# Performance work log

Measured on AMD Instinct MI355X. Metric: run time of the kernel, lower is better.

Reference implementation:

```python
import jax, jax.numpy as jnp
import numpy as np

MAX_STEPS = 8
COMMIT = 0.25
DECAY = 0.99
EPS = 1e-5


def gru_cell(x, h, W_ih, W_hh, b_ih, b_hh):
    # PyTorch GRU cell, gate order (r, z, n)
    gx = x @ W_ih.T + b_ih            # [B, 3H]
    gh = h @ W_hh.T + b_hh            # [B, 3H]
    xr, xz, xn = jnp.split(gx, 3, axis=-1)
    hr, hz, hn = jnp.split(gh, 3, axis=-1)
    r = jax.nn.sigmoid(xr + hr)
    z = jax.nn.sigmoid(xz + hz)
    n = jnp.tanh(xn + r * hn)
    return (1.0 - z) * n + z * h


def setup_inputs() -> dict:
    key = jax.random.key(0)
    ks = jax.random.split(key, 16)
    B, C, Hs, Ws = 1024, 512, 7, 7
    D, K, Hd = 256, 8192, 512
    sc = lambda k, shape, s: (jax.random.normal(k, shape, jnp.float32) * s)
    codebook = jax.random.uniform(ks[14], (K, D), jnp.float32, -1.0 / K, 1.0 / K)
    return {
        "spatial_features": sc(ks[0], (B, C, Hs, Ws), 1.0),
        "bos_token": sc(ks[1], (D,), 0.02),
        "W_ih": sc(ks[2], (3 * Hd, D), 0.05),
        "W_hh": sc(ks[3], (3 * Hd, Hd), 0.05),
        "b_ih": sc(ks[4], (3 * Hd,), 0.05),
        "b_hh": sc(ks[5], (3 * Hd,), 0.05),
        "Wg": sc(ks[6], (C, Hd), 0.02),
        "bg": sc(ks[7], (C,), 0.02),
        "Wb": sc(ks[8], (C, Hd), 0.02),
        "bb": sc(ks[9], (C,), 0.02),
        "W1": sc(ks[10], (Hd, Hd + C), 0.03),
        "b1": sc(ks[11], (Hd,), 0.03),
        "W2": sc(ks[12], (D, Hd), 0.05),
        "b2": sc(ks[13], (D,), 0.05),
        "codebook": codebook,
        "ema_cluster_size": jnp.zeros((K,), jnp.float32),
        "ema_w": codebook,
    }


def reference(spatial_features, bos_token, W_ih, W_hh, b_ih, b_hh,
              Wg, bg, Wb, bb, W1, b1, W2, b2,
              codebook, ema_cluster_size, ema_w):
    B = spatial_features.shape[0]
    K, D = codebook.shape
    Hd = W_hh.shape[1]
    # FiLM + global mean pooling is linear -> fold mean over HxW once.
    # mean((1+g)*F + b) == (1+g)*mean(F) + b  (same math, fewer bytes)
    spatial_mean = spatial_features.mean(axis=(2, 3))  # [B, C]

    def step(carry, _):
        h, prev, cb, cs, ew, loss = carry
        h = gru_cell(prev, h, W_ih, W_hh, b_ih, b_hh)            # [B, Hd]
        gamma = h @ Wg.T + bg
        beta = h @ Wb.T + bb
        c = (1.0 + gamma) * spatial_mean + beta                   # [B, C]
        pin = jnp.concatenate([h, c], axis=-1)                    # [B, Hd+C]
        z = jax.nn.relu(pin @ W1.T + b1) @ W2.T + b2              # [B, D]
        # VQ nearest neighbor (squared L2)
        d = (jnp.sum(z * z, axis=-1, keepdims=True)
             - 2.0 * (z @ cb.T)
             + jnp.sum(cb * cb, axis=-1))                         # [B, K]
        idx = jnp.argmin(d, axis=-1)                              # [B]
        z_q = cb[idx]                                             # [B, D]
        # EMA codebook update (uses OLD codebook for this step's z_q)
        zd = jax.lax.stop_gradient(z)
        counts = jnp.zeros((K,), z.dtype).at[idx].add(1.0)
        dw = jnp.zeros_like(cb).at[idx].add(zd)
        cs = DECAY * cs + (1.0 - DECAY) * counts
        n_tot = cs.sum()
        cs = (cs + EPS) / (n_tot + K * EPS) * n_tot               # Laplace smoothing
        ew = DECAY * ew + (1.0 - DECAY) * dw
        cb_new = ew / cs[:, None]
        vq = COMMIT * jnp.mean((z - jax.lax.stop_gradient(z_q)) ** 2)
        z_q_ste = z + jax.lax.stop_gradient(z_q - z)              # straight-through
        return (h, z_q_ste, cb_new, cs, ew, loss + vq), (z_q_ste, idx, z)

    h0 = jnp.zeros((B, Hd), spatial_features.dtype)
    prev0 = jnp.broadcast_to(bos_token, (B, D))
    init = (h0, prev0, codebook, ema_cluster_size, ema_w, jnp.zeros((), jnp.float32))
    (h_final, _, _, _, _, total_loss), (codes, idxs, zc) = jax.lax.scan(
        step, init, None, length=MAX_STEPS)
    selected_codes = jnp.swapaxes(codes, 0, 1)   # [B, T, D]
    all_indices = jnp.swapaxes(idxs, 0, 1)       # [B, T]
    all_z_cont = jnp.swapaxes(zc, 0, 1)          # [B, T, D]
    avg_vq_loss = total_loss / MAX_STEPS
    return (h_final, selected_codes, all_indices, all_z_cont, avg_vq_loss)
```

## Files before the change

### kernel.cpp

```cpp
#include <hip/hip_runtime.h>

#define BATCH 1024
#define CDIM  512
#define DDIM  256
#define KCB   8192
#define HD    512
#define G3    1536
#define TSTEPS 8

#define WS_CB    ((size_t)0)
#define WS_EW    ((size_t)2097152)
#define WS_CSR   ((size_t)4194304)
#define WS_SM    ((size_t)6291456)
#define WS_H     ((size_t)6815744)
#define WS_PREV  ((size_t)7340032)
#define WS_Z     ((size_t)7602176)
#define WS_GX    ((size_t)7864320)
#define WS_GH    ((size_t)9437184)
#define WS_PIN   ((size_t)12058624)
#define WS_H1    ((size_t)13107200)
#define WS_CS    ((size_t)13631488)
#define WS_CBSQ  ((size_t)13639680)
#define WS_SZZ   ((size_t)13647872)
#define WS_NT    ((size_t)13657088)
#define WS_LOSS  ((size_t)13657090)
#define WS_IDX   ((size_t)13657092)
#define WS_ROWK  ((size_t)13658116)
#define WS_WGWB  ((size_t)13660164)
#define WS_BGBB  ((size_t)14184452)

#define OUT_HF    ((size_t)0)
#define OUT_CODES ((size_t)524288)
#define OUT_IDX   ((size_t)2621440)
#define OUT_ZC    ((size_t)2629632)
#define OUT_LOSS  ((size_t)4726784)

static __device__ __forceinline__ unsigned long long key32(float s, int col) {
  unsigned int u = __float_as_uint(s);
  u = (u & 0x80000000u) ? ~u : (u | 0x80000000u);
  return (((unsigned long long)u) << 32) | (unsigned long long)(unsigned int)col;
}

static __device__ __forceinline__ float pw128(const float* a) {
  float r0=a[0],r1=a[1],r2=a[2],r3=a[3],r4=a[4],r5=a[5],r6=a[6],r7=a[7];
  for (int i = 8; i < 128; i += 8) {
    r0+=a[i+0]; r1+=a[i+1]; r2+=a[i+2]; r3+=a[i+3];
    r4+=a[i+4]; r5+=a[i+5]; r6+=a[i+6]; r7+=a[i+7];
  }
  return ((r0+r1)+(r2+r3))+((r4+r5)+(r6+r7));
}

template<int BM,int BN,int BK,int TM,int TN>
__device__ __forceinline__ void gemm_engine(
    const float* __restrict__ A, int lda,
    const float* __restrict__ B, int ldb, int K,
    int m0, int n0, int tid,
    float* __restrict__ As, float* __restrict__ Bs,
    float (&acc)[TM][TN])
{
  constexpr int NT = 256;
  constexpr int K4 = BK/4;
  constexpr int LA = (BM*BK)/(4*NT);
  constexpr int LB = (BN*BK)/(4*NT);
  constexpr int SA = BM+4;
  constexpr int SB = BN+4;
  constexpr int ACW = (TM % 4 == 0) ? 4 : 2;
  constexpr int BCW = (TN % 4 == 0) ? 4 : 2;
  constexpr int ANC = TM/ACW;
  constexpr int BNC = TN/BCW;
  constexpr int AR  = BM/ANC;
  constexpr int BR  = BN/BNC;
  static_assert((BM/TM)*(BN/TN) == NT, "256 threads");
  static_assert(LA >= 1 && LB >= 1, "stage width");

  const int tx = tid % (BN/TN);
  const int ty = tid / (BN/TN);

  int arow[LA], ak4[LA], brow[LB], bk4[LB];
#pragma unroll
  for (int l=0;l<LA;++l){ int f=l*NT+tid; arow[l]=f/K4; ak4[l]=f%K4; }
#pragma unroll
  for (int l=0;l<LB;++l){ int f=l*NT+tid; brow[l]=f/K4; bk4[l]=f%K4; }

  float4 ra[LA], rb[LB];
#pragma unroll
  for (int l=0;l<LA;++l) ra[l] = *(const float4*)(A + (size_t)(m0+arow[l])*lda + ak4[l]*4);
#pragma unroll
  for (int l=0;l<LB;++l) rb[l] = *(const float4*)(B + (size_t)(n0+brow[l])*ldb + bk4[l]*4);
#pragma unroll
  for (int l=0;l<LA;++l){ int kb=ak4[l]*4, r=arow[l];
    As[(kb+0)*SA+r]=ra[l].x; As[(kb+1)*SA+r]=ra[l].y; As[(kb+2)*SA+r]=ra[l].z; As[(kb+3)*SA+r]=ra[l].w; }
#pragma unroll
  for (int l=0;l<LB;++l){ int kb=bk4[l]*4, r=brow[l];
    Bs[(kb+0)*SB+r]=rb[l].x; Bs[(kb+1)*SB+r]=rb[l].y; Bs[(kb+2)*SB+r]=rb[l].z; Bs[(kb+3)*SB+r]=rb[l].w; }
  __syncthreads();

  int cur = 0;
  for (int k0 = BK; k0 < K; k0 += BK) {
#pragma unroll
    for (int l=0;l<LA;++l) ra[l] = *(const float4*)(A + (size_t)(m0+arow[l])*lda + k0 + ak4[l]*4);
#pragma unroll
    for (int l=0;l<LB;++l) rb[l] = *(const float4*)(B + (size_t)(n0+brow[l])*ldb + k0 + bk4[l]*4);
    {
      const float* as = As + cur*(BK*SA);
      const float* bs = Bs + cur*(BK*SB);
#pragma unroll
      for (int kk=0;kk<BK;++kk){
        float af[TM], bf[TN];
#pragma unroll
        for (int c=0;c<ANC;++c){
          if constexpr (ACW == 4) {
            float4 v = *(const float4*)&as[kk*SA + c*AR + ty*4];
            af[c*4+0]=v.x; af[c*4+1]=v.y; af[c*4+2]=v.z; af[c*4+3]=v.w;
          } else {
            float2 v = *(const float2*)&as[kk*SA + c*AR + ty*2];
            af[c*2+0]=v.x; af[c*2+1]=v.y;
          }
        }
#pragma unroll
        for (int c=0;c<BNC;++c){
          if constexpr (BCW == 4) {
            float4 v = *(const float4*)&bs[kk*SB + c*BR + tx*4];
            bf[c*4+0]=v.x; bf[c*4+1]=v.y; bf[c*4+2]=v.z; bf[c*4+3]=v.w;
          } else {
            float2 v = *(const float2*)&bs[kk*SB + c*BR + tx*2];
            bf[c*2+0]=v.x; bf[c*2+1]=v.y;
          }
        }
#pragma unroll
        for (int i=0;i<TM;++i)
#pragma unroll
          for (int j=0;j<TN;++j) acc[i][j]=fmaf(af[i],bf[j],acc[i][j]);
      }
    }
    {
      float* as = As + (cur^1)*(BK*SA);
      float* bs = Bs + (cur^1)*(BK*SB);
#pragma unroll
      for (int l=0;l<LA;++l){ int kb=ak4[l]*4, r=arow[l];
        as[(kb+0)*SA+r]=ra[l].x; as[(kb+1)*SA+r]=ra[l].y; as[(kb+2)*SA+r]=ra[l].z; as[(kb+3)*SA+r]=ra[l].w; }
#pragma unroll
      for (int l=0;l<LB;++l){ int kb=bk4[l]*4, r=brow[l];
        bs[(kb+0)*SB+r]=rb[l].x; bs[(kb+1)*SB+r]=rb[l].y; bs[(kb+2)*SB+r]=rb[l].z; bs[(kb+3)*SB+r]=rb[l].w; }
    }
    __syncthreads();
    cur ^= 1;
  }
  {
    const float* as = As + cur*(BK*SA);
    const float* bs = Bs + cur*(BK*SB);
#pragma unroll
    for (int kk=0;kk<BK;++kk){
      float af[TM], bf[TN];
#pragma unroll
      for (int c=0;c<ANC;++c){
        if constexpr (ACW == 4) {
          float4 v = *(const float4*)&as[kk*SA + c*AR + ty*4];
          af[c*4+0]=v.x; af[c*4+1]=v.y; af[c*4+2]=v.z; af[c*4+3]=v.w;
        } else {
          float2 v = *(const float2*)&as[kk*SA + c*AR + ty*2];
          af[c*2+0]=v.x; af[c*2+1]=v.y;
        }
      }
#pragma unroll
      for (int c=0;c<BNC;++c){
        if constexpr (BCW == 4) {
          float4 v = *(const float4*)&bs[kk*SB + c*BR + tx*4];
          bf[c*4+0]=v.x; bf[c*4+1]=v.y; bf[c*4+2]=v.z; bf[c*4+3]=v.w;
        } else {
          float2 v = *(const float2*)&bs[kk*SB + c*BR + tx*2];
          bf[c*2+0]=v.x; bf[c*2+1]=v.y;
        }
      }
#pragma unroll
      for (int i=0;i<TM;++i)
#pragma unroll
        for (int j=0;j<TN;++j) acc[i][j]=fmaf(af[i],bf[j],acc[i][j]);
    }
  }
}

__global__ __launch_bounds__(256) void gemm_gxgh_kernel(
    const float* __restrict__ PREV, const float* __restrict__ H,
    const float* __restrict__ Wih, const float* __restrict__ Whh,
    const float* __restrict__ bih, const float* __restrict__ bhh,
    float* __restrict__ GX, float* __restrict__ GH)
{
  __shared__ float As[2*16*(64+4)];
  __shared__ float Bs[2*16*(64+4)];
  const int z = blockIdx.z;
  const float* A   = z ? H   : PREV;
  const float* B   = z ? Whh : Wih;
  const float* bia = z ? bhh : bih;
  float* C         = z ? GH  : GX;
  const int lda    = z ? HD  : DDIM;
  const int m0 = blockIdx.x * 64, n0 = blockIdx.y * 64;
  float acc[4][4] = {};
  gemm_engine<64,64,16,4,4>(A, lda, B, lda, lda, m0, n0, threadIdx.x, As, Bs, acc);
  {
#pragma clang fp contract(off)
    const int tx = threadIdx.x & 15, ty = threadIdx.x >> 4;
#pragma unroll
    for (int i = 0; i < 4; ++i)
#pragma unroll
      for (int j = 0; j < 4; ++j)
        C[(size_t)(m0 + ty*4 + i) * G3 + n0 + tx*4 + j] = acc[i][j] + bia[n0 + tx*4 + j];
  }
}

__global__ __launch_bounds__(256) void gemm_gb_film_kernel(
    const float* __restrict__ H, const float* __restrict__ W,
    const float* __restrict__ bv, const float* __restrict__ SM,
    float* __restrict__ PIN)
{
  __shared__ float As[2*32*(32+4)];
  __shared__ float Bs[2*32*(64+4)];
  const int m0 = blockIdx.x * 32, n0 = blockIdx.y * 64;
  float acc[2][4] = {};
  gemm_engine<32,64,32,2,4>(H, HD, W, HD, HD, m0, n0, threadIdx.x, As, Bs, acc);
  {
#pragma clang fp contract(off)
    const int tx = threadIdx.x & 15, ty = threadIdx.x >> 4;
    const int cb0 = n0 + tx * 4;
#pragma unroll
    for (int i = 0; i < 2; ++i) {
      const int row = m0 + ty*2 + i;
#pragma unroll
      for (int p = 0; p < 2; ++p) {
        float g  = acc[i][2*p]   + bv[cb0 + 2*p];
        float be = acc[i][2*p+1] + bv[cb0 + 2*p + 1];
        const int ch = (cb0 >> 1) + p;
        float t1 = 1.0f + g;
        float t2 = t1 * SM[(size_t)row * CDIM + ch];
        PIN[(size_t)row * 1024 + 512 + ch] = t2 + be;
      }
    }
  }
}

template<bool RELU,int BM,int BN,int BK,int TM,int TN>
__global__ __launch_bounds__(256) void gemm_mlp_kernel(
    const float* __restrict__ A, int lda,
    const float* __restrict__ B,
    const float* __restrict__ bias, int K, int N, float* __restrict__ C)
{
  __shared__ float As[2*BK*(BM+4)];
  __shared__ float Bs[2*BK*(BN+4)];
  const int m0 = blockIdx.x * BM, n0 = blockIdx.y * BN;
  float acc[TM][TN] = {};
  gemm_engine<BM,BN,BK,TM,TN>(A, lda, B, K, K, m0, n0, threadIdx.x, As, Bs, acc);
  {
#pragma clang fp contract(off)
    constexpr int ACW = (TM % 4 == 0) ? 4 : 2;
    constexpr int BCW = (TN % 4 == 0) ? 4 : 2;
    constexpr int AR  = BM/(TM/ACW);
    constexpr int BR  = BN/(TN/BCW);
    const int tx = threadIdx.x % (BN/TN), ty = threadIdx.x / (BN/TN);
#pragma unroll
    for (int i = 0; i < TM; ++i) {
      const int row = m0 + (i/ACW)*AR + ty*ACW + (i%ACW);
#pragma unroll
      for (int j = 0; j < TN; ++j) {
        const int col = n0 + (j/BCW)*BR + tx*BCW + (j%BCW);
        float v = acc[i][j] + bias[col];
        if (RELU) v = fmaxf(v, 0.0f);
        C[(size_t)row * N + col] = v;
      }
    }
  }
}

__global__ __launch_bounds__(256) void gemm_score_argmin(
    const float* __restrict__ A,
    const float* __restrict__ Bc,
    const float* __restrict__ cbsq,
    const float* __restrict__ szz,
    unsigned long long* __restrict__ rowkeys)
{
  __shared__ float As[16][68];
  __shared__ float Bs[16][68];
  __shared__ unsigned long long Ks[64][17];
  const int tid = threadIdx.x;
  const int tx = tid & 15, ty = tid >> 4;
  const int fid = blockIdx.x + (blockIdx.y << 4);
  const int xcd = fid & 7;
  const int loc = fid >> 3;
  const int m0 = (loc & 15) * 64;
  const int n0 = ((xcd << 4) + (loc >> 4)) * 64;
  const int lr = tid >> 2, lq = tid & 3;
  const float4* Ab = (const float4*)(A + (size_t)(m0 + lr) * DDIM);
  const float4* Bb = (const float4*)(Bc + (size_t)(n0 + lr) * DDIM);
  float acc[4][4] = {};
  for (int k0 = 0; k0 < DDIM; k0 += 16) {
    float4 av = Ab[(k0 >> 2) + lq];
    float4 bv = Bb[(k0 >> 2) + lq];
    __syncthreads();
    As[lq*4+0][lr] = av.x; As[lq*4+1][lr] = av.y;
    As[lq*4+2][lr] = av.z; As[lq*4+3][lr] = av.w;
    Bs[lq*4+0][lr] = bv.x; Bs[lq*4+1][lr] = bv.y;
    Bs[lq*4+2][lr] = bv.z; Bs[lq*4+3][lr] = bv.w;
    __syncthreads();
#pragma unroll
    for (int kk = 0; kk < 16; ++kk) {
      float4 a = *(const float4*)&As[kk][ty*4];
      float4 b = *(const float4*)&Bs[kk][tx*4];
      acc[0][0]=fmaf(a.x,b.x,acc[0][0]); acc[0][1]=fmaf(a.x,b.y,acc[0][1]); acc[0][2]=fmaf(a.x,b.z,acc[0][2]); acc[0][3]=fmaf(a.x,b.w,acc[0][3]);
      acc[1][0]=fmaf(a.y,b.x,acc[1][0]); acc[1][1]=fmaf(a.y,b.y,acc[1][1]); acc[1][2]=fmaf(a.y,b.z,acc[1][2]); acc[1][3]=fmaf(a.y,b.w,acc[1][3]);
      acc[2][0]=fmaf(a.z,b.x,acc[2][0]); acc[2][1]=fmaf(a.z,b.y,acc[2][1]); acc[2][2]=fmaf(a.z,b.z,acc[2][2]); acc[2][3]=fmaf(a.z,b.w,acc[2][3]);
      acc[3][0]=fmaf(a.w,b.x,acc[3][0]); acc[3][1]=fmaf(a.w,b.y,acc[3][1]); acc[3][2]=fmaf(a.w,b.z,acc[3][2]); acc[3][3]=fmaf(a.w,b.w,acc[3][3]);
    }
  }
  {
#pragma clang fp contract(off)
    const int nb = n0 + tx * 4;
#pragma unroll
    for (int i = 0; i < 4; ++i) {
      float sz = szz[m0 + ty*4 + i];
      unsigned long long kb[4];
#pragma unroll
      for (int j = 0; j < 4; ++j) {
        float g2 = 2.0f * acc[i][j];
        float t1 = sz - g2;
        float d  = t1 + cbsq[nb + j];
        kb[j] = key32(d, nb + j);
      }
      unsigned long long ka = kb[0] < kb[1] ? kb[0] : kb[1];
      unsigned long long kc = kb[2] < kb[3] ? kb[2] : kb[3];
      Ks[ty*4 + i][tx] = ka < kc ? ka : kc;
    }
  }
  __syncthreads();
  if (tid < 64) {
    unsigned long long best = Ks[tid][0];
#pragma unroll
    for (int t = 1; t < 16; ++t) {
      unsigned long long v = Ks[tid][t];
      best = v < best ? v : best;
    }
    atomicMin(&rowkeys[m0 + tid], best);
  }
}

__global__ __launch_bounds__(256) void pw256_rows_kernel(const float* __restrict__ src,
                                                         float* __restrict__ dst,
                                                         int square) {
#pragma clang fp contract(off)
  int gid = blockIdx.x * 256 + threadIdx.x;
  int row = gid >> 4;
  int l = gid & 15;
  const float* a = src + (size_t)row * 256 + ((l >> 3) << 7) + (l & 7);
  float v0 = a[0];
  float r = square ? v0 * v0 : v0;
  for (int i = 1; i < 16; ++i) {
    float w = a[i << 3];
    r += square ? w * w : w;
  }
  float t = r + __shfl_xor(r, 1);
  t = t + __shfl_xor(t, 2);
  t = t + __shfl_xor(t, 4);
  float s = t + __shfl_xor(t, 8);
  if (l == 0) dst[row] = s;
}

__global__ __launch_bounds__(256) void smean_kernel(const float* __restrict__ sf,
                                                    float* __restrict__ sm) {
#pragma clang fp contract(off)
  int i = blockIdx.x * 256 + threadIdx.x;
  const float* a = sf + (size_t)i * 49;
  float r0=a[0],r1=a[1],r2=a[2],r3=a[3],r4=a[4],r5=a[5],r6=a[6],r7=a[7];
  for (int k = 8; k < 48; k += 8) {
    r0+=a[k+0]; r1+=a[k+1]; r2+=a[k+2]; r3+=a[k+3];
    r4+=a[k+4]; r5+=a[k+5]; r6+=a[k+6]; r7+=a[k+7];
  }
  float res = ((r0+r1)+(r2+r3))+((r4+r5)+(r6+r7));
  res += a[48];
  sm[i] = res / 49.0f;
}

__global__ __launch_bounds__(256) void previnit_kernel(const float* __restrict__ bos,
                                                       float* __restrict__ prev) {
  int i = blockIdx.x * 256 + threadIdx.x;
  prev[i] = bos[i & (DDIM - 1)];
}

__global__ __launch_bounds__(256) void interleave_film_kernel(
    const float* __restrict__ Wg, const float* __restrict__ Wb,
    const float* __restrict__ bg, const float* __restrict__ bb,
    float* __restrict__ W, float* __restrict__ bv) {
  int i = blockIdx.x * 256 + threadIdx.x;
  int row = i >> 9, k = i & 511;
  const float* src = (row & 1) ? Wb : Wg;
  W[i] = src[(size_t)(row >> 1) * 512 + k];
  if (i < 1024) bv[i] = ((i & 1) ? bb : bg)[i >> 1];
}

__global__ __launch_bounds__(256) void gru_kernel(const float* __restrict__ gx,
                                                  const float* __restrict__ gh,
                                                  float* __restrict__ h,
                                                  float* __restrict__ pin) {
#pragma clang fp contract(off)
  int i = blockIdx.x * 256 + threadIdx.x;
  int b = i >> 9, j = i & 511;
  size_t o = (size_t)b * G3;
  float xr = gx[o + j], xz = gx[o + 512 + j], xn = gx[o + 1024 + j];
  float hr = gh[o + j], hz = gh[o + 512 + j], hn = gh[o + 1024 + j];
  float ar = xr + hr;
  float az = xz + hz;
  float er = expf(-ar);
  float ez = expf(-az);
  float r  = 1.0f / (1.0f + er);
  float zz = 1.0f / (1.0f + ez);
  float rh = r * hn;
  float an = xn + rh;
  float n  = tanhf(an);
  float hold = h[i];
  float t1 = (1.0f - zz) * n;
  float t2 = zz * hold;
  float hnew = t1 + t2;
  h[i] = hnew;
  pin[(size_t)b * 1024 + j] = hnew;
}

__global__ __launch_bounds__(256) void vq_apply_kernel(
    unsigned long long* __restrict__ rowkeys,
    const float* __restrict__ cb, const float* __restrict__ zbuf,
    float* __restrict__ prev, int* __restrict__ idxarr,
    float* __restrict__ loss_acc, float* __restrict__ out, int t)
{
#pragma clang fp contract(off)
  int b = blockIdx.x, d = threadIdx.x;
  int idx = (int)(rowkeys[b] & 0xFFFFFFFFull);
  float zq = cb[(size_t)idx * DDIM + d];
  float zb = zbuf[(size_t)b * DDIM + d];
  float delta = zq - zb;
  float zste = zb + delta;
  size_t td = ((size_t)b * TSTEPS + t) * DDIM + d;
  out[OUT_CODES + td] = zste;
  out[OUT_ZC + td] = zb;
  prev[(size_t)b * DDIM + d] = zste;
  if (d == 0) {
    idxarr[b] = idx;
    out[OUT_IDX + (size_t)b * TSTEPS + t] = (float)idx;
  }
  float diff = zb - zq;
  __shared__ float red[256];
  red[d] = diff * diff; __syncthreads();
  for (int s = 128; s > 0; s >>= 1) { if (d < s) red[d] += red[d + s]; __syncthreads(); }
  if (d == 0) {
    atomicAdd(loss_acc, red[0]);
    rowkeys[b] = ~0ULL;
  }
}

__global__ __launch_bounds__(1024) void csr_cs_kernel(const int* __restrict__ idxarr,
                                                      int* __restrict__ list,
                                                      int* __restrict__ base,
                                                      int* __restrict__ cnts,
                                                      float* __restrict__ cs,
                                                      float* __restrict__ nt) {
  __shared__ __align__(16) int sidx[BATCH];
  __shared__ int scnt[KCB];
  __shared__ int spart[1024];
  __shared__ float scs[KCB];
  __shared__ float s64v[64];
  const int t = threadIdx.x;
  sidx[t] = idxarr[t];
  for (int i = t; i < KCB; i += 1024) scnt[i] = 0;
  __syncthreads();
  const int my = sidx[t];
  atomicAdd(&scnt[my], 1);
  int rank = 0;
  {
    int b = 0;
    for (; b + 4 <= t; b += 4) {
      int4 v = *(const int4*)&sidx[b];
      rank += (v.x == my) + (v.y == my) + (v.z == my) + (v.w == my);
    }
    for (; b < t; ++b) rank += (sidx[b] == my) ? 1 : 0;
  }
  __syncthreads();
  const int c0 = t * 8;
  int loc[8]; int s0 = 0;
#pragma unroll
  for (int i = 0; i < 8; ++i) { loc[i] = s0; s0 += scnt[c0 + i]; }
  spart[t] = s0;
  __syncthreads();
  for (int off = 1; off < 1024; off <<= 1) {
    int v = (t >= off) ? spart[t - off] : 0;
    __syncthreads();
    spart[t] += v;
    __syncthreads();
  }
  {
    int incl = spart[t];
    __syncthreads();
    spart[t] = incl - s0;
    __syncthreads();
  }
  const int off = spart[t];
#pragma unroll
  for (int i = 0; i < 8; ++i) { base[c0 + i] = off + loc[i]; cnts[c0 + i] = scnt[c0 + i]; }
  const int kb = my >> 3, kr = my & 7;
  int bb = spart[kb];
  for (int i = 0; i < kr; ++i) bb += scnt[(kb << 3) + i];
  list[bb + rank] = t;

  {
#pragma clang fp contract(off)
    for (int i = t; i < KCB; i += 1024) {
      float a = 0.99f * cs[i];
      float b2 = 0.01f * (float)scnt[i];
      scs[i] = a + b2;
    }
    __syncthreads();
    if (t < 64) s64v[t] = pw128(scs + t * 128);
    __syncthreads();
    if (t == 0) {
      float v[64];
      for (int i = 0; i < 64; ++i) v[i] = s64v[i];
      for (int len = 64; len > 1; len >>= 1)
        for (int i = 0; i < (len >> 1); ++i) v[i] = v[2*i] + v[2*i+1];
      nt[0] = v[0];
      s64v[0] = v[0];
    }
    __syncthreads();
    const float n = s64v[0];
    const float den = n + 0.08192f;
    for (int i = t; i < KCB; i += 1024) {
      float t1 = scs[i] + 1e-5f;
      float q = t1 / den;
      cs[i] = q * n;
    }
  }
}

__global__ __launch_bounds__(256) void ema_fused_kernel(
    float* __restrict__ ew, const int* __restrict__ list,
    const int* __restrict__ base, const int* __restrict__ cnts,
    const float* __restrict__ zbuf, const float* __restrict__ cs,
    float* __restrict__ cb, float* __restrict__ cbsq)
{
#pragma clang fp contract(off)
  __shared__ float row2[256];
  __shared__ float ch[16];
  const int d = threadIdx.x;
  for (int r = 0; r < 8; ++r) {
    const int k = blockIdx.x * 8 + r;
    const int start = base[k], cnt = cnts[k];
    float acc = 0.0f;
    int i = 0;
    for (; i + 16 <= cnt; i += 16) {
      int bi[16];
#pragma unroll
      for (int u = 0; u < 16; ++u) bi[u] = list[start + i + u];
      float v[16];
#pragma unroll
      for (int u = 0; u < 16; ++u) v[u] = zbuf[(size_t)bi[u] * DDIM + d];
#pragma unroll
      for (int u = 0; u < 16; ++u) acc += v[u];
    }
    for (; i < cnt; ++i) {
      acc += zbuf[(size_t)list[start + i] * DDIM + d];
    }
    const size_t o = (size_t)k * DDIM + d;
    float a = 0.99f * ew[o];
    float bb = 0.01f * acc;
    float e = a + bb;
    ew[o] = e;
    float c = e / cs[k];
    cb[o] = c;
    row2[d] = c * c;
    __syncthreads();
    if (d < 16) {
      int h = d >> 3, j = d & 7;
      const float* p = row2 + h * 128 + j;
      float rr = p[0];
      for (int i2 = 1; i2 < 16; ++i2) rr += p[8 * i2];
      ch[d] = rr;
    }
    __syncthreads();
    if (d == 0) {
      float s0 = ((ch[0]+ch[1])+(ch[2]+ch[3]))+((ch[4]+ch[5])+(ch[6]+ch[7]));
      float s1 = ((ch[8]+ch[9])+(ch[10]+ch[11]))+((ch[12]+ch[13])+(ch[14]+ch[15]));
      cbsq[k] = s0 + s1;
    }
    __syncthreads();
  }
}

__global__ __launch_bounds__(256) void final_kernel(const float* __restrict__ h,
                                                    const float* __restrict__ loss_acc,
                                                    float* __restrict__ out) {
  int i = blockIdx.x * 256 + threadIdx.x;
  out[OUT_HF + i] = h[i];
  if (i == 0)
    out[OUT_LOSS] = 0.25f * (*loss_acc) / ((float)(BATCH * DDIM)) / (float)TSTEPS;
}

extern "C" void kernel_launch(void* const* d_in, const int* in_sizes, int n_in,
                              void* d_out, int out_size, void* d_ws, size_t ws_size,
                              hipStream_t stream) {
  const float* sf    = (const float*)d_in[0];
  const float* bos   = (const float*)d_in[1];
  const float* W_ih  = (const float*)d_in[2];
  const float* W_hh  = (const float*)d_in[3];
  const float* b_ih  = (const float*)d_in[4];
  const float* b_hh  = (const float*)d_in[5];
  const float* Wg    = (const float*)d_in[6];
  const float* bg    = (const float*)d_in[7];
  const float* Wb    = (const float*)d_in[8];
  const float* bb    = (const float*)d_in[9];
  const float* W1    = (const float*)d_in[10];
  const float* b1    = (const float*)d_in[11];
  const float* W2    = (const float*)d_in[12];
  const float* b2    = (const float*)d_in[13];
  const float* cb_in = (const float*)d_in[14];
  const float* cs_in = (const float*)d_in[15];
  const float* ew_in = (const float*)d_in[16];

  float* ws  = (float*)d_ws;
  float* out = (float*)d_out;

  float* CB   = ws + WS_CB;
  float* EW   = ws + WS_EW;
  int*   LIST = (int*)(ws + WS_CSR);
  int*   BASE = LIST + BATCH;
  int*   CNTS = BASE + KCB;
  float* SM   = ws + WS_SM;
  float* H    = ws + WS_H;
  float* PREV = ws + WS_PREV;
  float* Z    = ws + WS_Z;
  float* GX   = ws + WS_GX;
  float* GH   = ws + WS_GH;
  float* PIN  = ws + WS_PIN;
  float* H1   = ws + WS_H1;
  float* CS   = ws + WS_CS;
  float* CBSQ = ws + WS_CBSQ;
  float* SZZ  = ws + WS_SZZ;
  float* NT   = ws + WS_NT;
  float* LOSS = ws + WS_LOSS;
  int*   IDX  = (int*)(ws + WS_IDX);
  unsigned long long* ROWK = (unsigned long long*)(ws + WS_ROWK);
  float* WGWB = ws + WS_WGWB;
  float* BGBB = ws + WS_BGBB;

  (void)hipMemcpyAsync(CB, cb_in, (size_t)KCB * DDIM * 4, hipMemcpyDeviceToDevice, stream);
  (void)hipMemcpyAsync(EW, ew_in, (size_t)KCB * DDIM * 4, hipMemcpyDeviceToDevice, stream);
  (void)hipMemcpyAsync(CS, cs_in, (size_t)KCB * 4, hipMemcpyDeviceToDevice, stream);
  interleave_film_kernel<<<(1024*512)/256, 256, 0, stream>>>(Wg, Wb, bg, bb, WGWB, BGBB);
  (void)hipMemsetAsync(H, 0, (size_t)BATCH * HD * 4, stream);
  (void)hipMemsetAsync(LOSS, 0, 8, stream);
  (void)hipMemsetAsync(ROWK, 0xFF, BATCH * 8, stream);
  previnit_kernel<<<BATCH * DDIM / 256, 256, 0, stream>>>(bos, PREV);
  smean_kernel<<<BATCH * CDIM / 256, 256, 0, stream>>>(sf, SM);
  pw256_rows_kernel<<<(KCB * 16) / 256, 256, 0, stream>>>(CB, CBSQ, 1);

  for (int t = 0; t < TSTEPS; ++t) {
    gemm_gxgh_kernel<<<dim3(BATCH/64, G3/64, 2), 256, 0, stream>>>(
        PREV, H, W_ih, W_hh, b_ih, b_hh, GX, GH);
    gru_kernel<<<BATCH * HD / 256, 256, 0, stream>>>(GX, GH, H, PIN);

    gemm_gb_film_kernel<<<dim3(BATCH/32, 1024/64), 256, 0, stream>>>(H, WGWB, BGBB, SM, PIN);

    gemm_mlp_kernel<true, 64,32,32,4,2><<<dim3(BATCH/64, HD/32),   256, 0, stream>>>(PIN, 1024, W1, b1, 1024, HD, H1);
    gemm_mlp_kernel<false,32,32,32,2,2><<<dim3(BATCH/32, DDIM/32), 256, 0, stream>>>(H1, HD, W2, b2, HD, DDIM, Z);

    pw256_rows_kernel<<<(BATCH * 16) / 256, 256, 0, stream>>>(Z, SZZ, 1);
    gemm_score_argmin<<<dim3(BATCH/64, KCB/64), 256, 0, stream>>>(Z, CB, CBSQ, SZZ, ROWK);
    vq_apply_kernel<<<BATCH, 256, 0, stream>>>(ROWK, CB, Z, PREV, IDX, LOSS, out, t);

    csr_cs_kernel<<<1, 1024, 0, stream>>>(IDX, LIST, BASE, CNTS, CS, NT);
    ema_fused_kernel<<<KCB/8, 256, 0, stream>>>(EW, LIST, BASE, CNTS, Z, CS, CB, CBSQ);
  }

  final_kernel<<<BATCH * HD / 256, 256, 0, stream>>>(H, LOSS, out);
}
```

Baseline: 2.097 ms.

## Rebalance GRU gate GEMM grid and shrink MLP tiles; drop XCD swizzle in score GEMM

The two GRU gate GEMMs now share one flat grid. The input-side GEMM (K=256) keeps 64x64 tiles, while the hidden-side GEMM (K=512) uses 64x32 tiles with a deeper K step, so the longer-K work is split across more blocks. The first MLP GEMM moves to 32x32 tiles to raise the block count. The XCD-aware block remapping in the codebook score/argmin kernel is replaced by a plain 2D block index. Together these aim to improve load balance and occupancy across CUs, but dropping the swizzle may reduce L2 locality for codebook reads.

```diff
diff --git a/kernel.cpp b/kernel.cpp
--- a/kernel.cpp
+++ b/kernel.cpp
@@ -186,25 +186,35 @@
     const float* __restrict__ bih, const float* __restrict__ bhh,
     float* __restrict__ GX, float* __restrict__ GH)
 {
-  __shared__ float As[2*16*(64+4)];
-  __shared__ float Bs[2*16*(64+4)];
-  const int z = blockIdx.z;
-  const float* A   = z ? H   : PREV;
-  const float* B   = z ? Whh : Wih;
-  const float* bia = z ? bhh : bih;
-  float* C         = z ? GH  : GX;
-  const int lda    = z ? HD  : DDIM;
-  const int m0 = blockIdx.x * 64, n0 = blockIdx.y * 64;
-  float acc[4][4] = {};
-  gemm_engine<64,64,16,4,4>(A, lda, B, lda, lda, m0, n0, threadIdx.x, As, Bs, acc);
-  {
-#pragma clang fp contract(off)
-    const int tx = threadIdx.x & 15, ty = threadIdx.x >> 4;
-#pragma unroll
-    for (int i = 0; i < 4; ++i)
-#pragma unroll
-      for (int j = 0; j < 4; ++j)
-        C[(size_t)(m0 + ty*4 + i) * G3 + n0 + tx*4 + j] = acc[i][j] + bia[n0 + tx*4 + j];
+  __shared__ float As[2*32*(64+4)];
+  __shared__ float Bs[2*32*(32+4)];
+  const int m0 = blockIdx.x * 64;
+  if (blockIdx.y < 24) {
+    const int n0 = blockIdx.y * 64;
+    float acc[4][4] = {};
+    gemm_engine<64,64,16,4,4>(PREV, DDIM, Wih, DDIM, DDIM, m0, n0, threadIdx.x, As, Bs, acc);
+    {
+#pragma clang fp contract(off)
+      const int tx = threadIdx.x & 15, ty = threadIdx.x >> 4;
+#pragma unroll
+      for (int i = 0; i < 4; ++i)
+#pragma unroll
+        for (int j = 0; j < 4; ++j)
+          GX[(size_t)(m0 + ty*4 + i) * G3 + n0 + tx*4 + j] = acc[i][j] + bih[n0 + tx*4 + j];
+    }
+  } else {
+    const int n0 = (blockIdx.y - 24) * 32;
+    float acc[4][2] = {};
+    gemm_engine<64,32,32,4,2>(H, HD, Whh, HD, HD, m0, n0, threadIdx.x, As, Bs, acc);
+    {
+#pragma clang fp contract(off)
+      const int tx = threadIdx.x & 15, ty = threadIdx.x >> 4;
+#pragma unroll
+      for (int i = 0; i < 4; ++i)
+#pragma unroll
+        for (int j = 0; j < 2; ++j)
+          GH[(size_t)(m0 + ty*4 + i) * G3 + n0 + tx*2 + j] = acc[i][j] + bhh[n0 + tx*2 + j];
+    }
   }
 }
 
@@ -282,11 +292,7 @@
   __shared__ unsigned long long Ks[64][17];
   const int tid = threadIdx.x;
   const int tx = tid & 15, ty = tid >> 4;
-  const int fid = blockIdx.x + (blockIdx.y << 4);
-  const int xcd = fid & 7;
-  const int loc = fid >> 3;
-  const int m0 = (loc & 15) * 64;
-  const int n0 = ((xcd << 4) + (loc >> 4)) * 64;
+  const int m0 = blockIdx.x * 64, n0 = blockIdx.y * 64;
   const int lr = tid >> 2, lq = tid & 3;
   const float4* Ab = (const float4*)(A + (size_t)(m0 + lr) * DDIM);
   const float4* Bb = (const float4*)(Bc + (size_t)(n0 + lr) * DDIM);
@@ -656,13 +662,13 @@
   pw256_rows_kernel<<<(KCB * 16) / 256, 256, 0, stream>>>(CB, CBSQ, 1);
 
   for (int t = 0; t < TSTEPS; ++t) {
-    gemm_gxgh_kernel<<<dim3(BATCH/64, G3/64, 2), 256, 0, stream>>>(
+    gemm_gxgh_kernel<<<dim3(BATCH/64, 72), 256, 0, stream>>>(
         PREV, H, W_ih, W_hh, b_ih, b_hh, GX, GH);
     gru_kernel<<<BATCH * HD / 256, 256, 0, stream>>>(GX, GH, H, PIN);
 
     gemm_gb_film_kernel<<<dim3(BATCH/32, 1024/64), 256, 0, stream>>>(H, WGWB, BGBB, SM, PIN);
 
-    gemm_mlp_kernel<true, 64,32,32,4,2><<<dim3(BATCH/64, HD/32),   256, 0, stream>>>(PIN, 1024, W1, b1, 1024, HD, H1);
+    gemm_mlp_kernel<true, 32,32,32,2,2><<<dim3(BATCH/32, HD/32),   256, 0, stream>>>(PIN, 1024, W1, b1, 1024, HD, H1);
     gemm_mlp_kernel<false,32,32,32,2,2><<<dim3(BATCH/32, DDIM/32), 256, 0, stream>>>(H1, HD, W2, b2, HD, DDIM, Z);
 
     pw256_rows_kernel<<<(BATCH * 16) / 256, 256, 0, stream>>>(Z, SZZ, 1);
```

Measured after the change: 2.208 ms. +5.3%, slower.
